# Kernel optimization log

Measured on AMD Instinct MI355X. Metric: run time of the kernel, lower is better.

Reference implementation:

```python
import jax, jax.numpy as jnp
import numpy as np

HEIGHT = 32
SIGMA = 2.0
NUM_NEGATIVE = 4096
N, C = 32, 512
L = HEIGHT * HEIGHT


def _grid_weight(height: int, sigma: float) -> jnp.ndarray:
    # distance_weights: pairwise Euclidean distance between grid points
    ii, jj = np.meshgrid(np.arange(height), np.arange(height), indexing='ij')
    coords = np.stack([ii.ravel(), jj.ravel()], axis=1).astype(np.float32)  # [L, 2]
    d2 = ((coords[:, None, :] - coords[None, :, :]) ** 2).sum(-1)  # squared dist [L, L]
    w = -(0.5 / sigma ** 2) * d2
    np.fill_diagonal(w, -np.inf)
    return jax.nn.softmax(jnp.asarray(w, dtype=jnp.float32), axis=1)


def setup_inputs() -> dict:
    key = jax.random.key(0)
    k1, k2 = jax.random.split(key)
    embedding = jax.random.normal(k1, (N, L, C), dtype=jnp.float32)
    weight = _grid_weight(HEIGHT, SIGMA)  # [L, L] softmax-normalized grid kernel
    neg_indices = jax.random.randint(k2, (NUM_NEGATIVE,), 0, N * L, dtype=jnp.int64)
    return {"embedding": embedding, "weight": weight, "neg_indices": neg_indices}


def reference(embedding, weight, neg_indices):
    n, l, c = embedding.shape
    # F.normalize(dim=-1), eps=1e-12
    norm = jnp.maximum(jnp.linalg.norm(embedding, axis=-1, keepdims=True), 1e-12)
    e = embedding / norm  # [N, L, C]
    # target = weight @ e  (broadcast over batch)
    target = jnp.einsum('kl,nlc->nkc', weight, e)  # [N, L, C]
    sim_pos = jnp.sum(e * target, axis=-1)  # [N, L]
    flat = e.reshape(-1, c)  # [N*L, C]
    negatives = flat[neg_indices]  # [M, C]
    sim_neg = jnp.einsum('nlc,mc->nlm', e, negatives)  # [N, L, M]
    logits = jnp.concatenate([sim_pos[..., None], sim_neg], axis=2).reshape(n * l, 1 + neg_indices.shape[0])
    # CrossEntropyLoss with target class 0, mean reduction
    loss = -jnp.mean(jax.nn.log_softmax(logits, axis=-1)[:, 0])
    return loss
```

## Files before the change

### kernel.cpp

```cpp
#include <hip/hip_runtime.h>
#include <hip/hip_bf16.h>
#include <stdint.h>

#define L_DIM 1024
#define C_DIM 512
#define CB4 256
#define N_BATCH 32
#define M_NEG 4096
#define NROWS (N_BATCH * L_DIM)

typedef float f32x4 __attribute__((ext_vector_type(4)));
typedef int i32x4 __attribute__((ext_vector_type(4)));
typedef int i32x8 __attribute__((ext_vector_type(8)));

#define E4_SCALE 32.0f
#define MX_SCALE 122
#define FMT_FP4 4

template <int GOFF>
__device__ __forceinline__ void gl_lds16(const uint8_t* g, uint8_t* l) {
  __builtin_amdgcn_global_load_lds(
      (const __attribute__((address_space(1))) void*)g,
      (__attribute__((address_space(3))) void*)l, 16, GOFF, 0);
}

__device__ __forceinline__ uint32_t fp4_enc(float x) {
  const uint32_t s = (__float_as_uint(x) >> 31) << 3;
  const float a = fabsf(x);
  uint32_t c;
  c = a < 0.25f ? 0u
    : a < 0.75f ? 1u
    : a < 1.25f ? 2u
    : a < 1.75f ? 3u
    : a < 2.5f  ? 4u
    : a < 3.5f  ? 5u
    : a < 5.0f  ? 6u : 7u;
  return s | c;
}

__device__ __forceinline__ i32x8 fp4_op(i32x4 d) {
  return __builtin_shufflevector(d, d, 0, 1, 2, 3, -1, -1, -1, -1);
}

__device__ __forceinline__ int swz(int row) { return (row >> 1) & 3; }

__global__ __launch_bounds__(256) void k_normalize(const float* __restrict__ emb,
                                                   uint8_t* __restrict__ out,
                                                   float* __restrict__ zerobuf,
                                                   float* __restrict__ loss_out) {
  if (blockIdx.x < 256) zerobuf[blockIdx.x * 256 + threadIdx.x] = 0.0f;
  if (blockIdx.x == 0 && threadIdx.x == 0) loss_out[0] = 0.0f;
  const int lane = threadIdx.x & 63;
  const int wave = threadIdx.x >> 6;
  const long row = (long)blockIdx.x * 4 + wave;
  const float4* src = (const float4*)(emb + row * C_DIM);
  float4 v0 = src[2 * lane];
  float4 v1 = src[2 * lane + 1];
  float ss = v0.x * v0.x + v0.y * v0.y + v0.z * v0.z + v0.w * v0.w +
             v1.x * v1.x + v1.y * v1.y + v1.z * v1.z + v1.w * v1.w;
#pragma unroll
  for (int off = 1; off < 64; off <<= 1) ss += __shfl_xor(ss, off, 64);
  const float s = E4_SCALE / fmaxf(sqrtf(ss), 1e-12f);
  uint32_t pk = fp4_enc(v0.x * s)        | (fp4_enc(v0.y * s) << 4) |
                (fp4_enc(v0.z * s) << 8) | (fp4_enc(v0.w * s) << 12) |
                (fp4_enc(v1.x * s) << 16)| (fp4_enc(v1.y * s) << 20) |
                (fp4_enc(v1.z * s) << 24)| (fp4_enc(v1.w * s) << 28);
  ((uint32_t*)(out + row * CB4))[lane] = pk;
}

__global__ __launch_bounds__(256, 4) void k_gemm_fused(
    const uint8_t* __restrict__ E4, const int* __restrict__ idx,
    const float* __restrict__ W, float* __restrict__ rowsum,
    float* __restrict__ simpos) {
  __shared__ __align__(16) unsigned char smem_raw[20480];
  uint8_t* sA = (uint8_t*)smem_raw;
  uint8_t* sB = sA + 128 * 64;

  const int tid = threadIdx.x;
  const int lane = tid & 63;
  const int wave = tid >> 6;
  const int wm = wave >> 1, wn = wave & 1;
  const int q = lane >> 4, c16 = lane & 15;

  const int bid = blockIdx.x;
  const bool is0 = bid >= 2048;
  long rowBase, colBase, n = 0;
  if (is0) {
    const int t = bid - 2048;
    const int xcd = t & 7, slot = t >> 3;
    rowBase = (long)(xcd * 32 + (slot & 31)) * 128;
    colBase = (long)(slot >> 5) * 128;
  } else {
    const int xcd = bid & 7, slot = bid >> 3;
    n = xcd * 4 + (slot & 3);
    const int inner = slot >> 2;
    rowBase = (long)(inner & 7) * 128;
    colBase = (long)(inner >> 3) * 128;
  }
  const long aBase = is0 ? rowBase : n * L_DIM + rowBase;

  const uint8_t* pA[2];
  const uint8_t* pB[2];
#pragma unroll
  for (int r = 0; r < 2; ++r) {
    const int c = r * 256 + tid;
    const int rw = c >> 2, cb = c & 3;
    pA[r] = E4 + (aBase + rw) * CB4 + (cb ^ swz(rw)) * 16;
    const long bRow = is0 ? (long)idx[colBase + rw] : n * L_DIM + colBase + rw;
    pB[r] = E4 + bRow * CB4 + (cb ^ swz(rw)) * 16;
  }

  int ldsB[4], ldsA[4];
#pragma unroll
  for (int j = 0; j < 4; ++j) {
    const int rowB = wn * 64 + j * 16 + c16;
    ldsB[j] = rowB * 64 + (q ^ swz(rowB)) * 16;
    const int rowA = wm * 64 + j * 16 + c16;
    ldsA[j] = rowA * 64 + (q ^ swz(rowA)) * 16;
  }

  f32x4 acc[4][4] = {};

  auto kstep = [&]() {
    __syncthreads();
    i32x8 bfr[4];
#pragma unroll
    for (int j = 0; j < 4; ++j)
      bfr[j] = fp4_op(*(const i32x4*)(sB + ldsB[j]));
#pragma unroll
    for (int i = 0; i < 4; ++i) {
      i32x8 af = fp4_op(*(const i32x4*)(sA + ldsA[i]));
#pragma unroll
      for (int j = 0; j < 4; ++j)
        acc[i][j] = __builtin_amdgcn_mfma_scale_f32_16x16x128_f8f6f4(
            af, bfr[j], acc[i][j], FMT_FP4, FMT_FP4,
            0, MX_SCALE, 0, MX_SCALE);
    }
    __syncthreads();
  };

  gl_lds16<0>(pA[0], sA + tid * 16);
  gl_lds16<0>(pA[1], sA + (256 + tid) * 16);
  gl_lds16<0>(pB[0], sB + tid * 16);
  gl_lds16<0>(pB[1], sB + (256 + tid) * 16);
  kstep();
  gl_lds16<64>(pA[0], sA + tid * 16);
  gl_lds16<64>(pA[1], sA + (256 + tid) * 16);
  gl_lds16<64>(pB[0], sB + tid * 16);
  gl_lds16<64>(pB[1], sB + (256 + tid) * 16);
  kstep();
  gl_lds16<128>(pA[0], sA + tid * 16);
  gl_lds16<128>(pA[1], sA + (256 + tid) * 16);
  gl_lds16<128>(pB[0], sB + tid * 16);
  gl_lds16<128>(pB[1], sB + (256 + tid) * 16);
  kstep();
  gl_lds16<192>(pA[0], sA + tid * 16);
  gl_lds16<192>(pA[1], sA + (256 + tid) * 16);
  gl_lds16<192>(pB[0], sB + tid * 16);
  gl_lds16<192>(pB[1], sB + (256 + tid) * 16);
  kstep();

  if (is0) {
    float* S = (float*)smem_raw;
#pragma unroll
    for (int i = 0; i < 4; ++i)
#pragma unroll
      for (int r = 0; r < 4; ++r) {
        const float s = __expf(acc[i][0][r]) + __expf(acc[i][1][r]) +
                        __expf(acc[i][2][r]) + __expf(acc[i][3][r]);
        S[wave * 1280 + (i * 16 + q * 4 + r) * 20 + c16] = s;
      }
    __syncthreads();
    if (tid < 128) {
      const int wm2 = tid >> 6, row64 = tid & 63;
      const float* p0 = (const float*)S + (wm2 * 2 + 0) * 1280 + row64 * 20;
      const float* p1 = (const float*)S + (wm2 * 2 + 1) * 1280 + row64 * 20;
      float4 t0 = ((const float4*)p0)[0], t1 = ((const float4*)p0)[1];
      float4 t2 = ((const float4*)p0)[2], t3 = ((const float4*)p0)[3];
      float4 u0 = ((const float4*)p1)[0], u1 = ((const float4*)p1)[1];
      float4 u2 = ((const float4*)p1)[2], u3 = ((const float4*)p1)[3];
      float v = t0.x + t0.y + t0.z + t0.w + t1.x + t1.y + t1.z + t1.w +
                t2.x + t2.y + t2.z + t2.w + t3.x + t3.y + t3.z + t3.w +
                u0.x + u0.y + u0.z + u0.w + u1.x + u1.y + u1.z + u1.w +
                u2.x + u2.y + u2.z + u2.w + u3.x + u3.y + u3.z + u3.w;
      atomicAdd(&rowsum[rowBase + tid], v);
    }
  } else {
    float* G = (float*)smem_raw;
#pragma unroll
    for (int p = 0; p < 4; ++p) {
      if (wm == (p >> 1)) {
#pragma unroll
        for (int ii = 0; ii < 2; ++ii) {
          const int i = (p & 1) * 2 + ii;
#pragma unroll
          for (int j = 0; j < 4; ++j)
#pragma unroll
            for (int r = 0; r < 4; ++r)
              G[(ii * 16 + q * 4 + r) * 132 + wn * 64 + j * 16 + c16] =
                  acc[i][j][r];
        }
      }
      __syncthreads();
      {
        const int rr = tid >> 3;
        const int chunk = tid & 7;
        const long krow = rowBase + p * 32 + rr;
        float v = 0.0f;
#pragma unroll
        for (int u = 0; u < 4; ++u) {
          const float4 g =
              *(const float4*)(G + rr * 132 + chunk * 16 + u * 4);
          const float4 w4 = *(const float4*)(W + krow * L_DIM + colBase +
                                             chunk * 16 + u * 4);
          v += g.x * w4.x + g.y * w4.y + g.z * w4.z + g.w * w4.w;
        }
        v += __shfl_xor(v, 1, 64);
        v += __shfl_xor(v, 2, 64);
        v += __shfl_xor(v, 4, 64);
        if (chunk == 0) atomicAdd(&simpos[n * L_DIM + krow], v);
      }
      __syncthreads();
    }
  }
}

__global__ __launch_bounds__(256) void k_finalize(const float* __restrict__ rowsum,
                                                  const float* __restrict__ simpos,
                                                  float* __restrict__ out) {
  const int gid = blockIdx.x * 256 + threadIdx.x;
  const float sp = simpos[gid];
  float v = __logf(rowsum[gid] + __expf(sp)) - sp;
#pragma unroll
  for (int off = 1; off < 64; off <<= 1) v += __shfl_xor(v, off, 64);
  __shared__ float ws[4];
  if ((threadIdx.x & 63) == 0) ws[threadIdx.x >> 6] = v;
  __syncthreads();
  if (threadIdx.x == 0)
    atomicAdd(out, (ws[0] + ws[1] + ws[2] + ws[3]) * (1.0f / (float)NROWS));
}

extern "C" void kernel_launch(void* const* d_in, const int* in_sizes, int n_in,
                              void* d_out, int out_size, void* d_ws, size_t ws_size,
                              hipStream_t stream) {
  const float* emb = (const float*)d_in[0];
  const float* weight = (const float*)d_in[1];
  const int* negidx = (const int*)d_in[2];
  float* out = (float*)d_out;
  char* ws = (char*)d_ws;

  uint8_t* E4 = (uint8_t*)ws;
  float* rowsum = (float*)(ws + 8388608);
  float* simpos = (float*)(ws + 8519680);

  k_normalize<<<NROWS / 4, 256, 0, stream>>>(emb, E4, rowsum, out);
  k_gemm_fused<<<10240, 256, 0, stream>>>(E4, negidx, weight, rowsum, simpos);
  k_finalize<<<NROWS / 256, 256, 0, stream>>>(rowsum, simpos, out);
}
```

Baseline: 166.1 us.

## Issue all K-slice loads up front and wait per slice with vmcnt barriers

The GEMM kernel now issues all four K-slices of A and B tiles into a 64 KB LDS buffer at once. Each slice is consumed after a partial s_waitcnt vmcnt plus barrier, instead of the serialized load-sync-compute-sync sequence per slice. This overlaps global-to-LDS latency of later slices with MFMA work on earlier ones and removes several barriers. In exchange LDS use grows from 20 KB to 64 KB per block and the launch bound drops to 2 blocks per CU, reducing occupancy.

```diff
diff --git a/kernel.cpp b/kernel.cpp
--- a/kernel.cpp
+++ b/kernel.cpp
@@ -43,6 +43,8 @@
 }
 
 __device__ __forceinline__ int swz(int row) { return (row >> 1) & 3; }
+
+#define WAITK(n) asm volatile("s_waitcnt vmcnt(" #n ")\n\ts_barrier" ::: "memory")
 
 __global__ __launch_bounds__(256) void k_normalize(const float* __restrict__ emb,
                                                    uint8_t* __restrict__ out,
@@ -68,13 +70,13 @@
   ((uint32_t*)(out + row * CB4))[lane] = pk;
 }
 
-__global__ __launch_bounds__(256, 4) void k_gemm_fused(
+__global__ __launch_bounds__(256, 2) void k_gemm_fused(
     const uint8_t* __restrict__ E4, const int* __restrict__ idx,
     const float* __restrict__ W, float* __restrict__ rowsum,
     float* __restrict__ simpos) {
-  __shared__ __align__(16) unsigned char smem_raw[20480];
+  __shared__ __align__(16) unsigned char smem_raw[65536];
   uint8_t* sA = (uint8_t*)smem_raw;
-  uint8_t* sB = sA + 128 * 64;
+  uint8_t* sB = sA + 32768;
 
   const int tid = threadIdx.x;
   const int lane = tid & 63;
@@ -121,44 +123,48 @@
 
   f32x4 acc[4][4] = {};
 
-  auto kstep = [&]() {
-    __syncthreads();
+  gl_lds16<0>(pA[0], sA + tid * 16);
+  gl_lds16<0>(pA[1], sA + (256 + tid) * 16);
+  gl_lds16<0>(pB[0], sB + tid * 16);
+  gl_lds16<0>(pB[1], sB + (256 + tid) * 16);
+  gl_lds16<64>(pA[0], sA + 8192 + tid * 16);
+  gl_lds16<64>(pA[1], sA + 8192 + (256 + tid) * 16);
+  gl_lds16<64>(pB[0], sB + 8192 + tid * 16);
+  gl_lds16<64>(pB[1], sB + 8192 + (256 + tid) * 16);
+  gl_lds16<128>(pA[0], sA + 16384 + tid * 16);
+  gl_lds16<128>(pA[1], sA + 16384 + (256 + tid) * 16);
+  gl_lds16<128>(pB[0], sB + 16384 + tid * 16);
+  gl_lds16<128>(pB[1], sB + 16384 + (256 + tid) * 16);
+  gl_lds16<192>(pA[0], sA + 24576 + tid * 16);
+  gl_lds16<192>(pA[1], sA + 24576 + (256 + tid) * 16);
+  gl_lds16<192>(pB[0], sB + 24576 + tid * 16);
+  gl_lds16<192>(pB[1], sB + 24576 + (256 + tid) * 16);
+
+  auto kcompute = [&](int kofs) {
     i32x8 bfr[4];
 #pragma unroll
     for (int j = 0; j < 4; ++j)
-      bfr[j] = fp4_op(*(const i32x4*)(sB + ldsB[j]));
+      bfr[j] = fp4_op(*(const i32x4*)(sB + kofs + ldsB[j]));
 #pragma unroll
     for (int i = 0; i < 4; ++i) {
-      i32x8 af = fp4_op(*(const i32x4*)(sA + ldsA[i]));
+      i32x8 af = fp4_op(*(const i32x4*)(sA + kofs + ldsA[i]));
 #pragma unroll
       for (int j = 0; j < 4; ++j)
         acc[i][j] = __builtin_amdgcn_mfma_scale_f32_16x16x128_f8f6f4(
             af, bfr[j], acc[i][j], FMT_FP4, FMT_FP4,
             0, MX_SCALE, 0, MX_SCALE);
     }
-    __syncthreads();
   };
 
-  gl_lds16<0>(pA[0], sA + tid * 16);
-  gl_lds16<0>(pA[1], sA + (256 + tid) * 16);
-  gl_lds16<0>(pB[0], sB + tid * 16);
-  gl_lds16<0>(pB[1], sB + (256 + tid) * 16);
-  kstep();
-  gl_lds16<64>(pA[0], sA + tid * 16);
-  gl_lds16<64>(pA[1], sA + (256 + tid) * 16);
-  gl_lds16<64>(pB[0], sB + tid * 16);
-  gl_lds16<64>(pB[1], sB + (256 + tid) * 16);
-  kstep();
-  gl_lds16<128>(pA[0], sA + tid * 16);
-  gl_lds16<128>(pA[1], sA + (256 + tid) * 16);
-  gl_lds16<128>(pB[0], sB + tid * 16);
-  gl_lds16<128>(pB[1], sB + (256 + tid) * 16);
-  kstep();
-  gl_lds16<192>(pA[0], sA + tid * 16);
-  gl_lds16<192>(pA[1], sA + (256 + tid) * 16);
-  gl_lds16<192>(pB[0], sB + tid * 16);
-  gl_lds16<192>(pB[1], sB + (256 + tid) * 16);
-  kstep();
+  WAITK(12);
+  kcompute(0);
+  WAITK(8);
+  kcompute(8192);
+  WAITK(4);
+  kcompute(16384);
+  WAITK(0);
+  kcompute(24576);
+  __syncthreads();
 
   if (is0) {
     float* S = (float*)smem_raw;
```

Result: slower. 180.8 us (+8.8%).
